# Kernel optimization log

Measured on AMD Instinct MI355X. Metric: run time of the kernel, lower is better.

Reference implementation:

```python
import jax, jax.numpy as jnp
import numpy as np

B, S, D = 2, 2048, 512
H, HD = 8, 64
MLP = 2048
WINDOW = 512          # sliding_window_size
N_GLOBAL = 64         # first N_GLOBAL tokens attend/are attended globally
NEG = -1e10


def _xavier(key, shape, fan_in, fan_out):
    lim = np.sqrt(6.0 / (fan_in + fan_out)).astype(np.float32)
    return jax.random.uniform(key, shape, jnp.float32, -lim, lim)


def setup_inputs() -> dict:
    key = jax.random.key(0)
    ks = jax.random.split(key, 8)
    inputs = jax.random.normal(ks[0], (B, S, D), jnp.float32)
    global_mask = jnp.zeros((B, S), jnp.bool_).at[:, :N_GLOBAL].set(True)
    return {
        "inputs": inputs,
        "global_mask": global_mask,
        "ln1_scale": jnp.ones((D,), jnp.float32),
        "ln1_bias": jnp.zeros((D,), jnp.float32),
        "wq": _xavier(ks[1], (D, H, HD), D, H * HD),
        "wk": _xavier(ks[2], (D, H, HD), D, H * HD),
        "wv": _xavier(ks[3], (D, H, HD), D, H * HD),
        "wo": _xavier(ks[4], (H, HD, D), H * HD, D),
        "ln2_scale": jnp.ones((D,), jnp.float32),
        "ln2_bias": jnp.zeros((D,), jnp.float32),
        "w1": _xavier(ks[5], (D, MLP), D, MLP),
        "b1": jnp.zeros((MLP,), jnp.float32),
        "w2": _xavier(ks[6], (MLP, D), MLP, D),
        "b2": jnp.zeros((D,), jnp.float32),
    }


def _layer_norm(x, scale, bias, eps=1e-6):
    m = jnp.mean(x, axis=-1, keepdims=True)
    v = jnp.mean(jnp.square(x - m), axis=-1, keepdims=True)
    return (x - m) * jax.lax.rsqrt(v + eps) * scale + bias


def _longformer_mask(global_mask, seq_len, window):
    # band: |i - j| <= window // 2  (sliding window)
    idx = jnp.arange(seq_len)
    band = jnp.abs(idx[:, None] - idx[None, :]) <= (window // 2)  # [S, S]
    # global rows OR global columns
    glob = global_mask[:, :, None] | global_mask[:, None, :]      # [B, S, S]
    return (band[None, :, :] | glob)[:, None, :, :]               # [B, 1, S, S]


def reference(inputs, global_mask, ln1_scale, ln1_bias, wq, wk, wv, wo,
              ln2_scale, ln2_bias, w1, b1, w2, b2):
    bsz, seq_len, _ = inputs.shape
    head_dim = wq.shape[-1]

    # --- pre-LN + Longformer self-attention ---
    x = _layer_norm(inputs, ln1_scale, ln1_bias)
    q = jnp.einsum('bsd,dhk->bshk', x, wq) / jnp.sqrt(jnp.float32(head_dim))
    k = jnp.einsum('bsd,dhk->bshk', x, wk)
    v = jnp.einsum('bsd,dhk->bshk', x, wv)

    mask = _longformer_mask(global_mask, seq_len, WINDOW)  # [B,1,S,S]
    scores = jnp.einsum('bqhk,bvhk->bhqv', q, k)           # [B,H,S,S]
    scores = jnp.where(mask, scores, NEG)
    attn = jax.nn.softmax(scores, axis=-1)
    ctx = jnp.einsum('bhqv,bvhk->bqhk', attn, v)
    attn_out = jnp.einsum('bqhk,hkd->bqd', ctx, wo)        # output proj, no bias

    x = attn_out + inputs  # residual (dropout deterministic -> identity)

    # --- pre-LN + MLP block ---
    y = _layer_norm(x, ln2_scale, ln2_bias)
    y = jax.nn.gelu(y @ w1 + b1) @ w2 + b2
    return x + y
```

## Files before the change

### kernel.cpp

```cpp
#include <hip/hip_runtime.h>
#include <hip/hip_bf16.h>

typedef __attribute__((ext_vector_type(4))) float f32x4;
typedef __bf16 bf16x8 __attribute__((ext_vector_type(8)));
using bf16 = __hip_bfloat16;

typedef __attribute__((address_space(1))) const void* gptr_t;
typedef __attribute__((address_space(3))) void* lptr_t;
typedef __attribute__((address_space(3))) char* lchar_t;

constexpr int BB = 2, SS = 2048, DDIM = 512, NHEAD = 8, HDIM = 64, MLPD = 2048;
constexpr int NTOK = BB * SS;
constexpr int WHALF = 256;
constexpr int NGLOB = 64;
constexpr float NEGBIG = -1e10f;

constexpr size_t SZ_X1    = (size_t)NTOK * DDIM * 2;
constexpr size_t SZ_WQKVT = (size_t)1536 * DDIM * 2;
constexpr size_t SZ_WOT   = (size_t)DDIM * DDIM * 2;
constexpr size_t SZ_W1T   = (size_t)MLPD * DDIM * 2;
constexpr size_t SZ_W2T   = (size_t)DDIM * MLPD * 2;
constexpr size_t SZ_HEAD  = (size_t)BB * NHEAD * SS * HDIM * 2;
constexpr size_t SZ_QKV   = 3 * SZ_HEAD;
constexpr size_t SZ_CTX   = (size_t)NTOK * DDIM * 2;
constexpr size_t SZ_XRES  = (size_t)NTOK * DDIM * 4;
constexpr size_t SZ_Y1    = (size_t)NTOK * DDIM * 2;
constexpr size_t SZ_H1    = (size_t)NTOK * MLPD * 2;

constexpr size_t OFF_X1    = 0;
constexpr size_t OFF_WQKVT = OFF_X1 + SZ_X1;
constexpr size_t OFF_WOT   = OFF_WQKVT + SZ_WQKVT;
constexpr size_t OFF_W1T   = OFF_WOT + SZ_WOT;
constexpr size_t OFF_W2T   = OFF_W1T + SZ_W1T;
constexpr size_t OFF_QKV   = OFF_W2T + SZ_W2T;
constexpr size_t OFF_CTX   = OFF_QKV + SZ_QKV;
constexpr size_t OFF_XRES  = OFF_CTX + SZ_CTX;
constexpr size_t OFF_Y1    = OFF_XRES + SZ_XRES;
constexpr size_t OFF_H1    = OFF_Y1 + SZ_Y1;
constexpr size_t OFF_GACC  = OFF_H1 + SZ_H1;
constexpr size_t OFF_GL    = OFF_GACC + (size_t)128 * 32 * 64 * 4;

struct TcEnt { const float* src; bf16* dst; int K, N, tiles_x, start; float scale; };
struct TcArgs { TcEnt e[6]; };

__global__ void transpose_cast_all(TcArgs a) {
  __shared__ __align__(16) bf16 tile[64][65];
  int bid = blockIdx.x;
  int wi = 5;
#pragma unroll
  for (int i = 4; i >= 0; --i)
    if (bid < a.e[i + 1].start) wi = i;
  const TcEnt& E = a.e[wi];
  int local = bid - E.start;
  int bx = local % E.tiles_x, by = local / E.tiles_x;
  int k0 = by * 64, n0 = bx * 64;
  int t = threadIdx.x;
  for (int it = 0; it < 16; ++it) {
    int idx = it * 256 + t;
    int r = idx >> 6, c = idx & 63;
    float v = E.src[(size_t)(k0 + r) * E.N + n0 + c] * E.scale;
    tile[c][r] = __float2bfloat16(v);
  }
  __syncthreads();
  for (int it = 0; it < 16; ++it) {
    int idx = it * 256 + t;
    int r = idx >> 6, c = idx & 63;
    E.dst[(size_t)(n0 + r) * E.K + k0 + c] = tile[r][c];
  }
}

__global__ void ln_kernel(const float* __restrict__ x, const float* __restrict__ sc,
                          const float* __restrict__ bi, bf16* __restrict__ out) {
  int wv = threadIdx.x >> 6;
  int lane = threadIdx.x & 63;
  int row = blockIdx.x * 4 + wv;
  const float* xr = x + (size_t)row * DDIM + lane * 8;
  float4 v0 = *(const float4*)(xr);
  float4 v1 = *(const float4*)(xr + 4);
  float vv[8] = {v0.x, v0.y, v0.z, v0.w, v1.x, v1.y, v1.z, v1.w};
  float s = 0.f;
  for (int i = 0; i < 8; ++i) s += vv[i];
  for (int m = 1; m < 64; m <<= 1) s += __shfl_xor(s, m, 64);
  float mean = s * (1.0f / DDIM);
  float vs = 0.f;
  for (int i = 0; i < 8; ++i) { float d = vv[i] - mean; vs += d * d; }
  for (int m = 1; m < 64; m <<= 1) vs += __shfl_xor(vs, m, 64);
  float rstd = rsqrtf(vs * (1.0f / DDIM) + 1e-6f);
  __align__(16) bf16 ov[8];
  int c0 = lane * 8;
  for (int i = 0; i < 8; ++i) {
    float y = (vv[i] - mean) * rstd * sc[c0 + i] + bi[c0 + i];
    ov[i] = __float2bfloat16(y);
  }
  *(uint4*)(&out[(size_t)row * DDIM + c0]) = *(const uint4*)ov;
}

template <int BM, int BN, int EPI>
__global__ __launch_bounds__(256, (BM + BN <= 128) ? 4 : ((BM + BN <= 192) ? 3 : 2))
void gemm_kernel(const bf16* __restrict__ A, const bf16* __restrict__ BT,
                 int M, int N, int K, int gx,
                 const float* __restrict__ ep_add, const float* __restrict__ ep_bias,
                 void* __restrict__ out0) {
  constexpr int AM = BM / 32;
  constexpr int AN = BN / 32;
  constexpr int CA4 = (BM / 8) / 4;
  constexpr int CB4 = (BN / 8) / 4;
  __shared__ __align__(16) bf16 As[2][BM][64];
  __shared__ __align__(16) bf16 Bs[2][BN][64];
  int t = threadIdx.x;
  int wv = t >> 6, lane = t & 63;
  int wr = wv >> 1, wc = wv & 1;
  int g = lane >> 4, lr = lane & 15;
  int sub_r = lane >> 3, sub_s = lane & 7;
  int nwg = gridDim.x;
  int bid = blockIdx.x;
  int swz = (bid & 7) * (nwg >> 3) + (bid >> 3);
  int m0 = (swz / gx) * BM;
  int n0 = (swz % gx) * BN;
  lchar_t asA = (lchar_t)&As[0][0][0];
  lchar_t asB = (lchar_t)&Bs[0][0][0];

  auto stage = [&](int kt, int bb) {
    int k0 = kt * 64;
#pragma unroll
    for (int i = 0; i < CA4; ++i) {
      int c = wv + 4 * i;
      int row = c * 8 + sub_r;
      int cb = sub_s ^ sub_r;
      __builtin_amdgcn_global_load_lds(
          (gptr_t)&A[(size_t)(m0 + row) * K + k0 + cb * 8],
          (lptr_t)(asA + bb * (BM * 128) + c * 1024), 16, 0, 0);
    }
#pragma unroll
    for (int i = 0; i < CB4; ++i) {
      int c = wv + 4 * i;
      int row = c * 8 + sub_r;
      int cb = sub_s ^ sub_r;
      __builtin_amdgcn_global_load_lds(
          (gptr_t)&BT[(size_t)(n0 + row) * K + k0 + cb * 8],
          (lptr_t)(asB + bb * (BN * 128) + c * 1024), 16, 0, 0);
    }
  };

  f32x4 acc[AM][AN] = {};
  int NT = K >> 6;
  stage(0, 0);
  asm volatile("s_waitcnt vmcnt(0)" ::: "memory");
  __builtin_amdgcn_s_barrier();
  __builtin_amdgcn_sched_barrier(0);
  for (int kt = 0; kt < NT; ++kt) {
    int bb = kt & 1;
    if (kt + 1 < NT) stage(kt + 1, bb ^ 1);
    const char* Ab = (const char*)&As[bb][0][0];
    const char* Bb = (const char*)&Bs[bb][0][0];
#pragma unroll
    for (int h = 0; h < 2; ++h) {
      bf16x8 af[AM], bfr[AN];
#pragma unroll
      for (int i = 0; i < AM; ++i) {
        int row = wr * (BM / 2) + i * 16 + lr;
        int sl = (h * 4 + g) ^ (row & 7);
        af[i] = *(const bf16x8*)(Ab + row * 128 + sl * 16);
      }
#pragma unroll
      for (int j = 0; j < AN; ++j) {
        int row = wc * (BN / 2) + j * 16 + lr;
        int sl = (h * 4 + g) ^ (row & 7);
        bfr[j] = *(const bf16x8*)(Bb + row * 128 + sl * 16);
      }
#pragma unroll
      for (int i = 0; i < AM; ++i)
#pragma unroll
        for (int j = 0; j < AN; ++j)
          acc[i][j] = __builtin_amdgcn_mfma_f32_16x16x32_bf16(af[i], bfr[j], acc[i][j], 0, 0, 0);
    }
    asm volatile("s_waitcnt vmcnt(0)" ::: "memory");
    __builtin_amdgcn_s_barrier();
    __builtin_amdgcn_sched_barrier(0);
  }
#pragma unroll
  for (int i = 0; i < AM; ++i)
#pragma unroll
    for (int j = 0; j < AN; ++j)
#pragma unroll
      for (int r = 0; r < 4; ++r) {
        int m = m0 + wr * (BM / 2) + i * 16 + g * 4 + r;
        int n = n0 + wc * (BN / 2) + j * 16 + lr;
        float val = acc[i][j][r];
        if constexpr (EPI == 0) {
          bf16* qkv = (bf16*)out0;
          int which = n >> 9;
          int hh = (n >> 6) & 7;
          int hd = n & 63;
          int b = m >> 11, sTok = m & 2047;
          size_t off;
          if (which == 2) {
            off = (size_t)2 * (BB * NHEAD * SS * HDIM) +
                  ((size_t)(b * NHEAD + hh) * HDIM + hd) * SS + sTok;
          } else {
            off = (size_t)which * (BB * NHEAD * SS * HDIM) +
                  ((size_t)(b * NHEAD + hh) * SS + sTok) * HDIM + hd;
          }
          qkv[off] = __float2bfloat16(val);
        } else if constexpr (EPI == 1) {
          ((float*)out0)[(size_t)m * N + n] = val + ep_add[(size_t)m * N + n];
        } else if constexpr (EPI == 2) {
          float xb = val + ep_bias[n];
          float u = 1.5957691216057308f * (xb + 0.044715f * xb * xb * xb);
          float ge = xb / (1.0f + __expf(-u));
          ((bf16*)out0)[(size_t)m * N + n] = __float2bfloat16(ge);
        } else {
          ((float*)out0)[(size_t)m * N + n] = val + ep_bias[n] + ep_add[(size_t)m * N + n];
        }
      }
}

constexpr int NBANDQ = (SS - NGLOB) / 32;
constexpr int NBAND7 = 16 * NBANDQ;
constexpr int NGSPL7 = 16 * 2 * 4;
constexpr int NWG7   = NBAND7 + NGSPL7;

__global__ __launch_bounds__(128, 2)
void attn_kernel(const bf16* __restrict__ Qb, const bf16* __restrict__ Kb,
                 const bf16* __restrict__ VTb, bf16* __restrict__ ctx,
                 float* __restrict__ gacc, float* __restrict__ gl) {
  __shared__ __align__(16) bf16 Ks[2][64][64];
  __shared__ __align__(16) bf16 Vs[2][64][64];
  __shared__ __align__(16) bf16 Plds[2][16][72];
  int t = threadIdx.x;
  int w = t >> 6, lane = t & 63;
  int g = lane >> 4, lr = lane & 15;
  int sub_r = lane >> 3, sub_s = lane & 7;
  int bid = blockIdx.x;
  int swz = (bid & 7) * (NWG7 / 8) + (bid >> 3);

  bool isBand = swz < NBAND7;
  int bh, qq0;
  int k0 = 0, sp = 0, qt = 0;
  if (isBand) {
    bh = swz / NBANDQ;
    qq0 = NGLOB + (swz % NBANDQ) * 32;
  } else {
    int gidx = swz - NBAND7;
    bh = gidx >> 3;
    qt = (gidx >> 2) & 1;
    sp = gidx & 3;
    qq0 = qt * 32;
    k0 = sp * (SS / 4);
  }
  int b = bh >> 3, h = bh & 7;
  const bf16* Qh = Qb + (size_t)bh * SS * HDIM;
  const bf16* Kh = Kb + (size_t)bh * SS * HDIM;
  const bf16* VTh = VTb + (size_t)bh * HDIM * SS;
  int qq0w = qq0 + w * 16;

  bf16x8 aq0 = *(const bf16x8*)&Qh[(size_t)(qq0w + lr) * HDIM + g * 8];
  bf16x8 aq1 = *(const bf16x8*)&Qh[(size_t)(qq0w + lr) * HDIM + 32 + g * 8];

  lchar_t ksB = (lchar_t)&Ks[0][0][0];
  lchar_t vsB = (lchar_t)&Vs[0][0][0];
  int cb = sub_s ^ sub_r;

  auto stageKV = [&](int kb, int bb) {
#pragma unroll
    for (int i = 0; i < 4; ++i) {
      int c = w * 4 + i;
      int row = c * 8 + sub_r;
      __builtin_amdgcn_global_load_lds(
          (gptr_t)&Kh[(size_t)(kb + row) * HDIM + cb * 8],
          (lptr_t)(ksB + bb * 8192 + c * 1024), 16, 0, 0);
      __builtin_amdgcn_global_load_lds(
          (gptr_t)&VTh[(size_t)row * SS + kb + cb * 8],
          (lptr_t)(vsB + bb * 8192 + c * 1024), 16, 0, 0);
    }
  };

  float lsum[4] = {0.f, 0.f, 0.f, 0.f};
  f32x4 accO[4] = {};
  const char* ksR = (const char*)&Ks[0][0][0];
  const char* vsR = (const char*)&Vs[0][0][0];

  auto computeT = [&](int kb, int bb, bool domask) {
    const char* Kb_ = ksR + bb * 8192;
    const char* Vb_ = vsR + bb * 8192;
    f32x4 s[4];
#pragma unroll
    for (int sub = 0; sub < 4; ++sub) {
      int row = sub * 16 + lr;
      int sl0 = g ^ (row & 7);
      int sl1 = (4 + g) ^ (row & 7);
      bf16x8 ka = *(const bf16x8*)(Kb_ + row * 128 + sl0 * 16);
      bf16x8 kc = *(const bf16x8*)(Kb_ + row * 128 + sl1 * 16);
      f32x4 z = {};
      z = __builtin_amdgcn_mfma_f32_16x16x32_bf16(aq0, ka, z, 0, 0, 0);
      z = __builtin_amdgcn_mfma_f32_16x16x32_bf16(aq1, kc, z, 0, 0, 0);
      s[sub] = z;
    }
    if (domask) {
#pragma unroll
      for (int sub = 0; sub < 4; ++sub)
#pragma unroll
        for (int r = 0; r < 4; ++r) {
          int i = qq0w + g * 4 + r;
          int d = i - (kb + sub * 16 + lr);
          bool ok = (unsigned)(d + WHALF) <= 2u * WHALF;
          s[sub][r] = ok ? s[sub][r] : NEGBIG;
        }
    }
    float p[4][4];
#pragma unroll
    for (int sub = 0; sub < 4; ++sub)
#pragma unroll
      for (int r = 0; r < 4; ++r) p[sub][r] = __expf(s[sub][r]);
#pragma unroll
    for (int r = 0; r < 4; ++r)
      lsum[r] += (p[0][r] + p[1][r]) + (p[2][r] + p[3][r]);
#pragma unroll
    for (int sub = 0; sub < 4; ++sub)
#pragma unroll
      for (int r = 0; r < 4; ++r)
        Plds[w][g * 4 + r][sub * 16 + lr] = __float2bfloat16(p[sub][r]);
    asm volatile("s_waitcnt lgkmcnt(0)" ::: "memory");
    __builtin_amdgcn_sched_barrier(0);
    bf16x8 paLo = *(const bf16x8*)&Plds[w][lr][g * 8];
    bf16x8 paHi = *(const bf16x8*)&Plds[w][lr][32 + g * 8];
#pragma unroll
    for (int dc = 0; dc < 4; ++dc) {
      int row = dc * 16 + lr;
      int slLo = g ^ (row & 7);
      int slHi = (4 + g) ^ (row & 7);
      bf16x8 vfLo = *(const bf16x8*)(Vb_ + row * 128 + slLo * 16);
      bf16x8 vfHi = *(const bf16x8*)(Vb_ + row * 128 + slHi * 16);
      accO[dc] = __builtin_amdgcn_mfma_f32_16x16x32_bf16(paLo, vfLo, accO[dc], 0, 0, 0);
      accO[dc] = __builtin_amdgcn_mfma_f32_16x16x32_bf16(paHi, vfHi, accO[dc], 0, 0, 0);
    }
  };

  int bs = 0, nt;
  if (isBand) {
    int blo = qq0 - WHALF;
    bs = (blo < NGLOB) ? NGLOB : (blo & ~63);
    int be = qq0 + 32 + WHALF;
    if (be > SS) be = SS;
    nt = 1 + ((be - bs + 63) >> 6);
  } else {
    nt = (SS / 4) / 64;
  }
  auto kb_of = [&](int i) {
    if (isBand) return (i == 0) ? 0 : bs + (i - 1) * 64;
    return k0 + i * 64;
  };

  stageKV(kb_of(0), 0);
  asm volatile("s_waitcnt vmcnt(0)" ::: "memory");
  __builtin_amdgcn_s_barrier();
  __builtin_amdgcn_sched_barrier(0);
  for (int i = 0; i < nt; ++i) {
    int bb = i & 1;
    if (i + 1 < nt) stageKV(kb_of(i + 1), bb ^ 1);
    int kb = kb_of(i);
    bool domask = isBand && (i > 0) &&
                  ((kb < qq0w - 241) || (kb + 63 > qq0w + WHALF));
    computeT(kb, bb, domask);
    asm volatile("s_waitcnt vmcnt(0)" ::: "memory");
    __builtin_amdgcn_s_barrier();
    __builtin_amdgcn_sched_barrier(0);
  }

#pragma unroll
  for (int m = 1; m < 16; m <<= 1)
#pragma unroll
    for (int r = 0; r < 4; ++r) lsum[r] += __shfl_xor(lsum[r], m, 64);

  if (isBand) {
#pragma unroll
    for (int r = 0; r < 4; ++r) {
      float rL = 1.0f / lsum[r];
      int m = b * SS + qq0w + g * 4 + r;
#pragma unroll
      for (int dc = 0; dc < 4; ++dc) {
        int col = h * HDIM + dc * 16 + lr;
        ctx[(size_t)m * DDIM + col] = __float2bfloat16(accO[dc][r] * rL);
      }
    }
  } else {
    int grp = ((bh * 2 + qt) * 4 + sp);
#pragma unroll
    for (int r = 0; r < 4; ++r) {
      int rowi = w * 16 + g * 4 + r;
#pragma unroll
      for (int dc = 0; dc < 4; ++dc)
        gacc[((size_t)grp * 32 + rowi) * 64 + dc * 16 + lr] = accO[dc][r];
      if (lr == 0) gl[grp * 32 + rowi] = lsum[r];
    }
  }
}

__global__ __launch_bounds__(64, 4)
void attn_combine_kernel(const float* __restrict__ gacc, const float* __restrict__ gl,
                         bf16* __restrict__ ctx) {
  int grp4 = blockIdx.x;
  int bh = grp4 >> 1, qt = grp4 & 1;
  int b = bh >> 3, h = bh & 7;
  int c = threadIdx.x;
  for (int r = 0; r < 32; ++r) {
    float L = 0.f, val = 0.f;
    for (int s2 = 0; s2 < 4; ++s2) {
      L += gl[(grp4 * 4 + s2) * 32 + r];
      val += gacc[((size_t)(grp4 * 4 + s2) * 32 + r) * 64 + c];
    }
    ctx[(size_t)(b * SS + qt * 32 + r) * DDIM + h * HDIM + c] = __float2bfloat16(val / L);
  }
}

extern "C" void kernel_launch(void* const* d_in, const int* in_sizes, int n_in,
                              void* d_out, int out_size, void* d_ws, size_t ws_size,
                              hipStream_t stream) {
  const float* inputs = (const float*)d_in[0];
  const float* ln1_s = (const float*)d_in[2];
  const float* ln1_b = (const float*)d_in[3];
  const float* wq = (const float*)d_in[4];
  const float* wk = (const float*)d_in[5];
  const float* wv = (const float*)d_in[6];
  const float* wo = (const float*)d_in[7];
  const float* ln2_s = (const float*)d_in[8];
  const float* ln2_b = (const float*)d_in[9];
  const float* w1 = (const float*)d_in[10];
  const float* b1 = (const float*)d_in[11];
  const float* w2 = (const float*)d_in[12];
  const float* b2 = (const float*)d_in[13];

  char* ws = (char*)d_ws;
  bf16* x1    = (bf16*)(ws + OFF_X1);
  bf16* wqkvT = (bf16*)(ws + OFF_WQKVT);
  bf16* woT   = (bf16*)(ws + OFF_WOT);
  bf16* w1T   = (bf16*)(ws + OFF_W1T);
  bf16* w2T   = (bf16*)(ws + OFF_W2T);
  bf16* qkv   = (bf16*)(ws + OFF_QKV);
  bf16* ctx   = (bf16*)(ws + OFF_CTX);
  float* xres = (float*)(ws + OFF_XRES);
  bf16* y1    = (bf16*)(ws + OFF_Y1);
  bf16* h1    = (bf16*)(ws + OFF_H1);
  float* gacc = (float*)(ws + OFF_GACC);
  float* gl   = (float*)(ws + OFF_GL);
  size_t headsz = (size_t)BB * NHEAD * SS * HDIM;

  TcArgs ta;
  ta.e[0] = {wq, wqkvT,                       512, 512,  8,   0, 0.125f};
  ta.e[1] = {wk, wqkvT + (size_t)512 * 512,   512, 512,  8,  64, 1.f};
  ta.e[2] = {wv, wqkvT + (size_t)1024 * 512,  512, 512,  8, 128, 1.f};
  ta.e[3] = {wo, woT,                         512, 512,  8, 192, 1.f};
  ta.e[4] = {w1, w1T,                         512, 2048, 32, 256, 1.f};
  ta.e[5] = {w2, w2T,                         2048, 512, 8, 512, 1.f};
  transpose_cast_all<<<768, 256, 0, stream>>>(ta);

  ln_kernel<<<NTOK / 4, 256, 0, stream>>>(inputs, ln1_s, ln1_b, x1);
  gemm_kernel<64, 128, 0><<<12 * 64, 256, 0, stream>>>(x1, wqkvT, NTOK, 1536, 512, 12, nullptr, nullptr, qkv);
  attn_kernel<<<NWG7, 128, 0, stream>>>(qkv, qkv + headsz, qkv + 2 * headsz, ctx, gacc, gl);
  attn_combine_kernel<<<32, 64, 0, stream>>>(gacc, gl, ctx);
  gemm_kernel<64, 64, 1><<<8 * 64, 256, 0, stream>>>(ctx, woT, NTOK, 512, 512, 8, inputs, nullptr, xres);
  ln_kernel<<<NTOK / 4, 256, 0, stream>>>(xres, ln2_s, ln2_b, y1);
  gemm_kernel<128, 128, 2><<<16 * 32, 256, 0, stream>>>(y1, w1T, NTOK, 2048, 512, 16, nullptr, b1, h1);
  gemm_kernel<64, 64, 3><<<8 * 64, 256, 0, stream>>>(h1, w2T, NTOK, 512, 2048, 8, xres, b2, (float*)d_out);
}
```

Measured before the change: 111.9 us.

## Widen attention workgroups to 64 queries and fuse LN1 into weight prep kernel

The attention kernel now runs 4 waves (256 threads) per workgroup, covering 64 query rows instead of 32. Each staged K/V tile is therefore reused by twice as many queries, and the band and global-split workgroup counts are halved. The global-row partial accumulators and the combine kernel are resized to match. Separately, the first layer norm is merged into the weight transpose/cast kernel to save one launch. The trade-off is fewer workgroups with more waves each, which may lower parallelism across CUs and pulls in a few extra masked keys per band tile.

```diff
diff --git a/kernel.cpp b/kernel.cpp
--- a/kernel.cpp
+++ b/kernel.cpp
@@ -38,34 +38,62 @@
 constexpr size_t OFF_Y1    = OFF_XRES + SZ_XRES;
 constexpr size_t OFF_H1    = OFF_Y1 + SZ_Y1;
 constexpr size_t OFF_GACC  = OFF_H1 + SZ_H1;
-constexpr size_t OFF_GL    = OFF_GACC + (size_t)128 * 32 * 64 * 4;
+constexpr size_t OFF_GL    = OFF_GACC + (size_t)64 * 64 * 64 * 4;
 
 struct TcEnt { const float* src; bf16* dst; int K, N, tiles_x, start; float scale; };
-struct TcArgs { TcEnt e[6]; };
-
-__global__ void transpose_cast_all(TcArgs a) {
+struct PrepArgs {
+  TcEnt e[6];
+  const float* x; const float* ln_s; const float* ln_b; bf16* ln_out;
+};
+
+__global__ void prep_kernel(PrepArgs a) {
   __shared__ __align__(16) bf16 tile[64][65];
   int bid = blockIdx.x;
-  int wi = 5;
-#pragma unroll
-  for (int i = 4; i >= 0; --i)
-    if (bid < a.e[i + 1].start) wi = i;
-  const TcEnt& E = a.e[wi];
-  int local = bid - E.start;
-  int bx = local % E.tiles_x, by = local / E.tiles_x;
-  int k0 = by * 64, n0 = bx * 64;
   int t = threadIdx.x;
-  for (int it = 0; it < 16; ++it) {
-    int idx = it * 256 + t;
-    int r = idx >> 6, c = idx & 63;
-    float v = E.src[(size_t)(k0 + r) * E.N + n0 + c] * E.scale;
-    tile[c][r] = __float2bfloat16(v);
-  }
-  __syncthreads();
-  for (int it = 0; it < 16; ++it) {
-    int idx = it * 256 + t;
-    int r = idx >> 6, c = idx & 63;
-    E.dst[(size_t)(n0 + r) * E.K + k0 + c] = tile[r][c];
+  if (bid < 768) {
+    int wi = 5;
+#pragma unroll
+    for (int i = 4; i >= 0; --i)
+      if (bid < a.e[i + 1].start) wi = i;
+    const TcEnt& E = a.e[wi];
+    int local = bid - E.start;
+    int bx = local % E.tiles_x, by = local / E.tiles_x;
+    int k0 = by * 64, n0 = bx * 64;
+    for (int it = 0; it < 16; ++it) {
+      int idx = it * 256 + t;
+      int r = idx >> 6, c = idx & 63;
+      float v = E.src[(size_t)(k0 + r) * E.N + n0 + c] * E.scale;
+      tile[c][r] = __float2bfloat16(v);
+    }
+    __syncthreads();
+    for (int it = 0; it < 16; ++it) {
+      int idx = it * 256 + t;
+      int r = idx >> 6, c = idx & 63;
+      E.dst[(size_t)(n0 + r) * E.K + k0 + c] = tile[r][c];
+    }
+  } else {
+    int wv = t >> 6;
+    int lane = t & 63;
+    int row = (bid - 768) * 4 + wv;
+    const float* xr = a.x + (size_t)row * DDIM + lane * 8;
+    float4 v0 = *(const float4*)(xr);
+    float4 v1 = *(const float4*)(xr + 4);
+    float vv[8] = {v0.x, v0.y, v0.z, v0.w, v1.x, v1.y, v1.z, v1.w};
+    float s = 0.f;
+    for (int i = 0; i < 8; ++i) s += vv[i];
+    for (int m = 1; m < 64; m <<= 1) s += __shfl_xor(s, m, 64);
+    float mean = s * (1.0f / DDIM);
+    float vs = 0.f;
+    for (int i = 0; i < 8; ++i) { float d = vv[i] - mean; vs += d * d; }
+    for (int m = 1; m < 64; m <<= 1) vs += __shfl_xor(vs, m, 64);
+    float rstd = rsqrtf(vs * (1.0f / DDIM) + 1e-6f);
+    __align__(16) bf16 ov[8];
+    int c0 = lane * 8;
+    for (int i = 0; i < 8; ++i) {
+      float y = (vv[i] - mean) * rstd * a.ln_s[c0 + i] + a.ln_b[c0 + i];
+      ov[i] = __float2bfloat16(y);
+    }
+    *(uint4*)(&a.ln_out[(size_t)row * DDIM + c0]) = *(const uint4*)ov;
   }
 }
 
@@ -215,37 +243,35 @@
       }
 }
 
-constexpr int NBANDQ = (SS - NGLOB) / 32;
-constexpr int NBAND7 = 16 * NBANDQ;
-constexpr int NGSPL7 = 16 * 2 * 4;
-constexpr int NWG7   = NBAND7 + NGSPL7;
-
-__global__ __launch_bounds__(128, 2)
+constexpr int NBANDQ = (SS - NGLOB) / 64;
+constexpr int NBAND8 = 16 * NBANDQ;
+constexpr int NGSPL8 = 16 * 4;
+constexpr int NWG8   = NBAND8 + NGSPL8;
+
+__global__ __launch_bounds__(256, 2)
 void attn_kernel(const bf16* __restrict__ Qb, const bf16* __restrict__ Kb,
                  const bf16* __restrict__ VTb, bf16* __restrict__ ctx,
                  float* __restrict__ gacc, float* __restrict__ gl) {
   __shared__ __align__(16) bf16 Ks[2][64][64];
   __shared__ __align__(16) bf16 Vs[2][64][64];
-  __shared__ __align__(16) bf16 Plds[2][16][72];
+  __shared__ __align__(16) bf16 Plds[4][16][72];
   int t = threadIdx.x;
   int w = t >> 6, lane = t & 63;
   int g = lane >> 4, lr = lane & 15;
   int sub_r = lane >> 3, sub_s = lane & 7;
   int bid = blockIdx.x;
-  int swz = (bid & 7) * (NWG7 / 8) + (bid >> 3);
-
-  bool isBand = swz < NBAND7;
-  int bh, qq0;
-  int k0 = 0, sp = 0, qt = 0;
+  int swz = (bid & 7) * (NWG8 / 8) + (bid >> 3);
+
+  bool isBand = swz < NBAND8;
+  int bh, qq0, k0 = 0, sp = 0;
   if (isBand) {
     bh = swz / NBANDQ;
-    qq0 = NGLOB + (swz % NBANDQ) * 32;
+    qq0 = NGLOB + (swz % NBANDQ) * 64;
   } else {
-    int gidx = swz - NBAND7;
-    bh = gidx >> 3;
-    qt = (gidx >> 2) & 1;
+    int gidx = swz - NBAND8;
+    bh = gidx >> 2;
     sp = gidx & 3;
-    qq0 = qt * 32;
+    qq0 = 0;
     k0 = sp * (SS / 4);
   }
   int b = bh >> 3, h = bh & 7;
@@ -263,8 +289,8 @@
 
   auto stageKV = [&](int kb, int bb) {
 #pragma unroll
-    for (int i = 0; i < 4; ++i) {
-      int c = w * 4 + i;
+    for (int i = 0; i < 2; ++i) {
+      int c = w + 4 * i;
       int row = c * 8 + sub_r;
       __builtin_amdgcn_global_load_lds(
           (gptr_t)&Kh[(size_t)(kb + row) * HDIM + cb * 8],
@@ -340,7 +366,7 @@
   if (isBand) {
     int blo = qq0 - WHALF;
     bs = (blo < NGLOB) ? NGLOB : (blo & ~63);
-    int be = qq0 + 32 + WHALF;
+    int be = qq0 + 64 + WHALF;
     if (be > SS) be = SS;
     nt = 1 + ((be - bs + 63) >> 6);
   } else {
@@ -384,14 +410,14 @@
       }
     }
   } else {
-    int grp = ((bh * 2 + qt) * 4 + sp);
+    int grp = bh * 4 + sp;
 #pragma unroll
     for (int r = 0; r < 4; ++r) {
       int rowi = w * 16 + g * 4 + r;
 #pragma unroll
       for (int dc = 0; dc < 4; ++dc)
-        gacc[((size_t)grp * 32 + rowi) * 64 + dc * 16 + lr] = accO[dc][r];
-      if (lr == 0) gl[grp * 32 + rowi] = lsum[r];
+        gacc[((size_t)grp * 64 + rowi) * 64 + dc * 16 + lr] = accO[dc][r];
+      if (lr == 0) gl[grp * 64 + rowi] = lsum[r];
     }
   }
 }
@@ -399,17 +425,16 @@
 __global__ __launch_bounds__(64, 4)
 void attn_combine_kernel(const float* __restrict__ gacc, const float* __restrict__ gl,
                          bf16* __restrict__ ctx) {
-  int grp4 = blockIdx.x;
-  int bh = grp4 >> 1, qt = grp4 & 1;
+  int bh = blockIdx.x;
   int b = bh >> 3, h = bh & 7;
   int c = threadIdx.x;
-  for (int r = 0; r < 32; ++r) {
+  for (int r = 0; r < 64; ++r) {
     float L = 0.f, val = 0.f;
     for (int s2 = 0; s2 < 4; ++s2) {
-      L += gl[(grp4 * 4 + s2) * 32 + r];
-      val += gacc[((size_t)(grp4 * 4 + s2) * 32 + r) * 64 + c];
-    }
-    ctx[(size_t)(b * SS + qt * 32 + r) * DDIM + h * HDIM + c] = __float2bfloat16(val / L);
+      L += gl[(bh * 4 + s2) * 64 + r];
+      val += gacc[((size_t)(bh * 4 + s2) * 64 + r) * 64 + c];
+    }
+    ctx[(size_t)(b * SS + r) * DDIM + h * HDIM + c] = __float2bfloat16(val / L);
   }
 }
 
@@ -445,19 +470,19 @@
   float* gl   = (float*)(ws + OFF_GL);
   size_t headsz = (size_t)BB * NHEAD * SS * HDIM;
 
-  TcArgs ta;
-  ta.e[0] = {wq, wqkvT,                       512, 512,  8,   0, 0.125f};
-  ta.e[1] = {wk, wqkvT + (size_t)512 * 512,   512, 512,  8,  64, 1.f};
-  ta.e[2] = {wv, wqkvT + (size_t)1024 * 512,  512, 512,  8, 128, 1.f};
-  ta.e[3] = {wo, woT,                         512, 512,  8, 192, 1.f};
-  ta.e[4] = {w1, w1T,                         512, 2048, 32, 256, 1.f};
-  ta.e[5] = {w2, w2T,                         2048, 512, 8, 512, 1.f};
-  transpose_cast_all<<<768, 256, 0, stream>>>(ta);
-
-  ln_kernel<<<NTOK / 4, 256, 0, stream>>>(inputs, ln1_s, ln1_b, x1);
+  PrepArgs pa;
+  pa.e[0] = {wq, wqkvT,                       512, 512,  8,   0, 0.125f};
+  pa.e[1] = {wk, wqkvT + (size_t)512 * 512,   512, 512,  8,  64, 1.f};
+  pa.e[2] = {wv, wqkvT + (size_t)1024 * 512,  512, 512,  8, 128, 1.f};
+  pa.e[3] = {wo, woT,                         512, 512,  8, 192, 1.f};
+  pa.e[4] = {w1, w1T,                         512, 2048, 32, 256, 1.f};
+  pa.e[5] = {w2, w2T,                         2048, 512, 8, 512, 1.f};
+  pa.x = inputs; pa.ln_s = ln1_s; pa.ln_b = ln1_b; pa.ln_out = x1;
+  prep_kernel<<<768 + NTOK / 4, 256, 0, stream>>>(pa);
+
   gemm_kernel<64, 128, 0><<<12 * 64, 256, 0, stream>>>(x1, wqkvT, NTOK, 1536, 512, 12, nullptr, nullptr, qkv);
-  attn_kernel<<<NWG7, 128, 0, stream>>>(qkv, qkv + headsz, qkv + 2 * headsz, ctx, gacc, gl);
-  attn_combine_kernel<<<32, 64, 0, stream>>>(gacc, gl, ctx);
+  attn_kernel<<<NWG8, 256, 0, stream>>>(qkv, qkv + headsz, qkv + 2 * headsz, ctx, gacc, gl);
+  attn_combine_kernel<<<16, 64, 0, stream>>>(gacc, gl, ctx);
   gemm_kernel<64, 64, 1><<<8 * 64, 256, 0, stream>>>(ctx, woT, NTOK, 512, 512, 8, inputs, nullptr, xres);
   ln_kernel<<<NTOK / 4, 256, 0, stream>>>(xres, ln2_s, ln2_b, y1);
   gemm_kernel<128, 128, 2><<<16 * 32, 256, 0, stream>>>(y1, w1T, NTOK, 2048, 512, 16, nullptr, b1, h1);
```

Result: faster. 109.5 us (-2.1%).
